# Kernel tuning notes

Hardware: AMD Instinct MI355X
Metric: run time of the kernel (lower is better)

The kernel has to match this reference:

```python
import math
import jax, jax.numpy as jnp
import numpy as np

NUM_HEADS = 16
NUM_BUCKETS = 32
MAX_DISTANCE = 128
NEG_INF = -1e9
LN_EPS = 1e-5


def _rel_pos_bias(rab_emb, T):
    # buckets for relative position (i - j) clamped at 0, T5-style log buckets
    i = jnp.arange(T)[:, None]
    j = jnp.arange(T)[None, :]
    n = jnp.clip(i - j, 0, None)  # = -(mem - ctx), clamped min 0
    max_exact = NUM_BUCKETS // 2
    large = max_exact + (
        jnp.log(n.astype(jnp.float32) / max_exact + 1e-6)
        / math.log(MAX_DISTANCE / max_exact)
        * (NUM_BUCKETS - max_exact)
    ).astype(jnp.int32)
    large = jnp.minimum(large, NUM_BUCKETS - 1)
    buckets = jnp.where(n < max_exact, n, large)  # [T, T]
    return rab_emb[buckets].transpose(2, 0, 1)[None]  # [1, H, T, T]


def setup_inputs() -> dict:
    key = jax.random.key(0)
    ks = jax.random.split(key, 8)
    B, T, D = 2, 1024, 1024
    x = jax.random.normal(ks[0], (B, T, D), dtype=jnp.float32)
    # additive causal mask: 0 where allowed, -1e9 where blocked (code tests ==0 for allowed)
    causal_block = jnp.triu(jnp.ones((T, T), dtype=bool), k=1)
    attention_mask = jnp.where(causal_block, NEG_INF, 0.0).astype(jnp.float32)
    # key padding: second sequence has last 256 positions padded
    lengths = jnp.array([T, T - 256])
    key_padding_mask = jnp.arange(T)[None, :] >= lengths[:, None]  # True = pad
    s = 1.0 / math.sqrt(D)
    W_in = jax.random.normal(ks[1], (4 * D, D), dtype=jnp.float32) * s
    b_in = jax.random.normal(ks[2], (4 * D,), dtype=jnp.float32) * 0.02
    W_out = jax.random.normal(ks[3], (D, D), dtype=jnp.float32) * s
    b_out = jax.random.normal(ks[4], (D,), dtype=jnp.float32) * 0.02
    gamma = jnp.ones((D,), dtype=jnp.float32)
    beta = jnp.zeros((D,), dtype=jnp.float32)
    rab_emb = jax.random.normal(ks[5], (NUM_BUCKETS, NUM_HEADS), dtype=jnp.float32) * 0.02
    return {
        "x": x,
        "attention_mask": attention_mask,
        "key_padding_mask": key_padding_mask,
        "W_in": W_in,
        "b_in": b_in,
        "W_out": W_out,
        "b_out": b_out,
        "gamma": gamma,
        "beta": beta,
        "rab_emb": rab_emb,
    }


def reference(x, attention_mask, key_padding_mask, W_in, b_in, W_out, b_out, gamma, beta, rab_emb):
    B, T, D = x.shape
    H = NUM_HEADS
    hd = D // H
    alpha = hd ** (-0.5)

    h = jax.nn.silu(x @ W_in.T + b_in)  # [B, T, 4D]
    U, V, Q, K = jnp.split(h, 4, axis=-1)

    def heads(t):
        return t.reshape(B, T, H, hd).transpose(0, 2, 1, 3)  # [B, H, T, hd]

    Qh, Kh, Vh = heads(Q), heads(K), heads(V)

    rab = _rel_pos_bias(rab_emb, T)  # [1, H, T, T]
    logits = jnp.einsum("bhtd,bhsd->bhts", Qh, Kh) * alpha + rab + attention_mask[None, None]

    valid = (~key_padding_mask).astype(jnp.float32)[:, None, None, :]  # [B,1,1,T]
    allowed = (attention_mask == 0).astype(jnp.float32)[None, None] * valid  # [B,1,T,T] bcast
    # padded keys: torch masked_fill(-inf) then logits_safe -> -1e9
    logits = jnp.where(valid == 0, NEG_INF, logits)

    denom = jnp.clip(jnp.sum(allowed, axis=-1, keepdims=True), 1.0, None)
    attention = jax.nn.silu(logits) / denom  # pointwise SiLU attention, no softmax

    AV = jnp.einsum("bhts,bhsd->bthd", attention, Vh).reshape(B, T, D)

    mu = jnp.mean(AV, axis=-1, keepdims=True)
    var = jnp.var(AV, axis=-1, keepdims=True)
    normed = (AV - mu) / jnp.sqrt(var + LN_EPS) * gamma + beta

    y = (normed * U) @ W_out.T + b_out  # U_flat == U (head reshape round-trips)
    return x + y
```

## Files before the change

kernel.cpp:

```cpp
#include <hip/hip_runtime.h>
#include <stdint.h>

#define DEV static __device__ __forceinline__

typedef unsigned short u16;
typedef float floatx4 __attribute__((ext_vector_type(4)));
typedef short bf16x8 __attribute__((ext_vector_type(8)));

constexpr int Tn = 1024;
constexpr int Dn = 1024;
constexpr int Hn = 16;
constexpr int FD = 4096;

DEV float b2f(u16 u) { union { unsigned int i; float f; } v; v.i = ((unsigned int)u) << 16; return v.f; }
DEV u16 f2b(float f) {
  union { float f; unsigned int i; } v; v.f = f;
  unsigned int x = v.i;
  x += 0x7fffu + ((x >> 16) & 1u);
  return (u16)(x >> 16);
}

DEV void async16(const void* g, void* l) {
  __builtin_amdgcn_global_load_lds((const __attribute__((address_space(1))) void*)g,
                                   (__attribute__((address_space(3))) void*)l,
                                   16, 0, 0);
}

DEV bool is_bf16(const unsigned* gdet) { return gdet[0] == 0x3F803F80u; }
DEV int kp_mode(const unsigned* kp) {
  unsigned d511 = kp[511];
  if (d511 == 0x01010101u) return 1;
  unsigned d1023 = kp[1023];
  if (d1023 == 0x3F803F80u) return 2;
  unsigned d2047 = kp[2047];
  return (d2047 == 0x3F800000u) ? 3 : 0;
}
DEV int nchunks(int qt) { return (qt < 6) ? 1 : ((qt < 12) ? 2 : 3); }

__global__ void prep_all(const void* __restrict__ x, const void* __restrict__ wi,
                         const void* __restrict__ wo, u16* __restrict__ xb,
                         u16* __restrict__ wib, u16* __restrict__ wob,
                         const void* __restrict__ bi, const void* __restrict__ bo,
                         const void* __restrict__ ga, const void* __restrict__ be,
                         const void* __restrict__ kp, const void* __restrict__ rab,
                         float* __restrict__ smallf, float* __restrict__ biasG,
                         float* __restrict__ denomG, unsigned long long* __restrict__ kmaskG)
{
  const unsigned* gdet = (const unsigned*)ga;
  const int bid = blockIdx.x;
  const int tid = threadIdx.x;
  __shared__ unsigned char vb[1024];
  __shared__ int wtot[4];

  if (bid < 1792) {
    if (is_bf16(gdet)) return;
    int i0 = bid * 256 + tid;
#pragma unroll
    for (int k = 0; k < 4; k++) {
      int i = i0 + k * 458752;
      const void* src; u16* dst; int j;
      if (i < 524288)       { src = x;  dst = xb;  j = i; }
      else if (i < 1572864) { src = wi; dst = wib; j = i - 524288; }
      else                  { src = wo; dst = wob; j = i - 1572864; }
      float4 v = ((const float4*)src)[j];
      ushort4 o; o.x = f2b(v.x); o.y = f2b(v.y); o.z = f2b(v.z); o.w = f2b(v.w);
      ((ushort4*)dst)[j] = o;
    }
    return;
  }
  if (bid < 1794) {
    const int b = bid - 1792;
    const int mode = kp_mode((const unsigned*)kp);
    int vv[4];
    const int t0 = tid * 4;
#pragma unroll
    for (int i = 0; i < 4; i++) {
      int t = b * Tn + t0 + i;
      int pad;
      if (mode == 0)      pad = (((const int*)kp)[t] != 0);
      else if (mode == 1) pad = (((const unsigned char*)kp)[t] != 0);
      else if (mode == 2) pad = (((const u16*)kp)[t] != 0);
      else                pad = (((const float*)kp)[t] != 0.f);
      vv[i] = pad ? 0 : 1;
      vb[t0 + i] = (unsigned char)vv[i];
    }
    int p1 = vv[0], p2 = p1 + vv[1], p3 = p2 + vv[2], p4 = p3 + vv[3];
    const int lane = tid & 63, w = tid >> 6;
    int ws = p4;
#pragma unroll
    for (int off = 1; off < 64; off <<= 1) {
      int t = __shfl_up(ws, off, 64);
      if (lane >= off) ws += t;
    }
    if (lane == 63) wtot[w] = ws;
    __syncthreads();
    int base = 0;
    for (int j = 0; j < w; j++) base += wtot[j];
    int excl = base + ws - p4;
    int c1 = excl + p1, c2 = excl + p2, c3 = excl + p3, c4 = excl + p4;
    denomG[b * Tn + t0 + 0] = (float)(c1 < 1 ? 1 : c1);
    denomG[b * Tn + t0 + 1] = (float)(c2 < 1 ? 1 : c2);
    denomG[b * Tn + t0 + 2] = (float)(c3 < 1 ? 1 : c3);
    denomG[b * Tn + t0 + 3] = (float)(c4 < 1 ? 1 : c4);
    if (tid < 16) {
      unsigned long long m = 0;
      for (int j = 0; j < 64; j++) m |= (unsigned long long)vb[tid * 64 + j] << j;
      kmaskG[b * 16 + tid] = m;
    }
    return;
  }
  const bool fbf = is_bf16(gdet);
  for (int i = tid; i < 7168; i += 256) {
    const void* src; int j;
    if (i < 4096)      { src = bi; j = i; }
    else if (i < 5120) { src = bo; j = i - 4096; }
    else if (i < 6144) { src = ga; j = i - 5120; }
    else               { src = be; j = i - 6144; }
    smallf[i] = fbf ? b2f(((const u16*)src)[j]) : ((const float*)src)[j];
  }
  for (int i = tid; i < Hn * Tn; i += 256) {
    int hh = i >> 10, d = i & 1023;
    int bk;
    if (d < 16) bk = d;
    else {
      float lg = logf((float)d * 0.0625f + 1e-6f) / logf(8.f) * 16.f;
      bk = 16 + (int)lg;
      bk = bk < 31 ? bk : 31;
    }
    int j = bk * Hn + hh;
    biasG[i] = fbf ? b2f(((const u16*)rab)[j]) : ((const float*)rab)[j];
  }
}

template<int BM, int BN, int WR, int WC, int EPI>
__global__ __launch_bounds__(WR * WC * 64, 2)
void gemm_bt(const u16* __restrict__ Ac, const u16* __restrict__ Ar,
             const u16* __restrict__ Bc, const u16* __restrict__ Br,
             const float* __restrict__ biasf, void* __restrict__ C,
             u16* __restrict__ VtG, const unsigned* __restrict__ gdet,
             int M, int N, int K)
{
  constexpr int NT = WR * WC * 64;
  __shared__ u16 As[BM * 64];
  __shared__ u16 Bs[BN * 64];
  const int fbf = is_bf16(gdet) ? 1 : 0;
  const u16* A  = fbf ? Ar : Ac;
  const u16* Bm = fbf ? Br : Bc;
  const int tid = threadIdx.x;
  const int lane = tid & 63;
  const int w = tid >> 6;
  const int wm = w / WC, wn = w % WC;
  const int q = lane >> 4, l16 = lane & 15;
  const int rowBase = blockIdx.y * BM;
  const int colBase = blockIdx.x * BN;
  const int ksl = K / gridDim.z;
  const int kb0 = blockIdx.z * ksl;

  floatx4 acc[4][4];
#pragma unroll
  for (int i = 0; i < 4; i++)
#pragma unroll
    for (int j = 0; j < 4; j++)
#pragma unroll
      for (int r = 0; r < 4; r++) acc[i][j][r] = 0.f;

  for (int kb = kb0; kb < kb0 + ksl; kb += 64) {
    __syncthreads();
#pragma unroll
    for (int i = 0; i < BM * 8 / NT; i++) {
      int c = i * NT + tid;
      int row = c >> 3, cl = (c & 7) ^ (row & 7);
      async16(&A[(size_t)(rowBase + row) * K + kb + cl * 8], &As[c * 8]);
    }
#pragma unroll
    for (int i = 0; i < BN * 8 / NT; i++) {
      int c = i * NT + tid;
      int row = c >> 3, cl = (c & 7) ^ (row & 7);
      async16(&Bm[(size_t)(colBase + row) * K + kb + cl * 8], &Bs[c * 8]);
    }
    __syncthreads();
    bf16x8 af[2][4], bfr[2][4];
    const int rsw = l16 & 7;
#pragma unroll
    for (int ko = 0; ko < 2; ko++) {
#pragma unroll
      for (int mt = 0; mt < 4; mt++) {
        int row = wm * 64 + mt * 16 + l16;
        af[ko][mt] = *(const bf16x8*)&As[(row * 8 + ((ko * 4 + q) ^ rsw)) * 8];
      }
#pragma unroll
      for (int nt = 0; nt < 4; nt++) {
        int row = wn * 64 + nt * 16 + l16;
        bfr[ko][nt] = *(const bf16x8*)&Bs[(row * 8 + ((ko * 4 + q) ^ rsw)) * 8];
      }
    }
#pragma unroll
    for (int ko = 0; ko < 2; ko++)
#pragma unroll
      for (int mt = 0; mt < 4; mt++)
#pragma unroll
        for (int nt = 0; nt < 4; nt++)
          acc[mt][nt] = __builtin_amdgcn_mfma_f32_16x16x32_bf16(af[ko][mt], bfr[ko][nt], acc[mt][nt], 0, 0, 0);
  }

  const bool isV = (EPI == 0) && (colBase >= Dn) && (colBase < 2 * Dn);
  const size_t pOff = (size_t)blockIdx.z * M * N;
#pragma unroll
  for (int mt = 0; mt < 4; mt++)
#pragma unroll
    for (int nt = 0; nt < 4; nt++) {
      int col = colBase + wn * 64 + nt * 16 + l16;
      float bcol = (EPI == 0) ? biasf[col] : 0.f;
      int row0 = rowBase + wm * 64 + mt * 16 + q * 4;
      if (EPI == 0) {
        u16 pr[4];
#pragma unroll
        for (int r = 0; r < 4; r++) {
          float v = acc[mt][nt][r] + bcol;
          v = v / (1.f + __expf(-v));
          pr[r] = f2b(v);
        }
        if (isV) {
          int d = col - Dn;
          u16* vp = &VtG[(((size_t)(row0 >> 10) * Hn + (d >> 6)) * 64 + (d & 63)) * Tn + (row0 & 1023)];
          *(uint2*)vp = make_uint2(pr[0] | ((unsigned)pr[1] << 16),
                                   pr[2] | ((unsigned)pr[3] << 16));
        } else {
#pragma unroll
          for (int r = 0; r < 4; r++)
            ((u16*)C)[(size_t)(row0 + r) * N + col] = pr[r];
        }
      } else {
#pragma unroll
        for (int r = 0; r < 4; r++)
          ((float*)C)[pOff + (size_t)(row0 + r) * N + col] = acc[mt][nt][r];
      }
    }
}

__global__ __launch_bounds__(256)
void reduce2(const float* __restrict__ Gp, const void* __restrict__ X,
             const float* __restrict__ bout, void* __restrict__ out,
             const unsigned* __restrict__ gdet)
{
  const int fbf = is_bf16(gdet) ? 1 : 0;
  const int row = blockIdx.x;
  const int tid = threadIdx.x;
  const size_t ridx = (size_t)row * Dn;
  float4 a = ((const float4*)(Gp + ridx))[tid];
#pragma unroll
  for (int ks = 1; ks < 4; ks++) {
    float4 p = ((const float4*)(Gp + (size_t)ks * 2097152 + ridx))[tid];
    a.x += p.x; a.y += p.y; a.z += p.z; a.w += p.w;
  }
  float4 bb = ((const float4*)bout)[tid];
  a.x += bb.x; a.y += bb.y; a.z += bb.z; a.w += bb.w;
  if (fbf) {
    ushort4 xv = ((const ushort4*)X)[ridx / 4 + tid];
    a.x += b2f(xv.x); a.y += b2f(xv.y); a.z += b2f(xv.z); a.w += b2f(xv.w);
    ushort4 o; o.x = f2b(a.x); o.y = f2b(a.y); o.z = f2b(a.z); o.w = f2b(a.w);
    ((ushort4*)out)[ridx / 4 + tid] = o;
  } else {
    float4 xv = ((const float4*)X)[ridx / 4 + tid];
    a.x += xv.x; a.y += xv.y; a.z += xv.z; a.w += xv.w;
    ((float4*)out)[ridx / 4 + tid] = a;
  }
}

__global__ __launch_bounds__(256, 4)
void attn_kern(const u16* __restrict__ h, const u16* __restrict__ VtG,
               const float* __restrict__ biasG, const float* __restrict__ denomG,
               const unsigned long long* __restrict__ kmaskG,
               float* __restrict__ AV)
{
  __shared__ u16 Qs[4096];
  __shared__ u16 Ks[4096];
  __shared__ u16 Vs[4096];
  __shared__ u16 Ps[4096];
  __shared__ float biasL[1024];
  const int tid = threadIdx.x;
  const int lane = tid & 63;
  const int w = tid >> 6;
  const int q = lane >> 4, l16 = lane & 15;

  int qt = 0, rem = blockIdx.x;
  for (;;) { int P = nchunks(qt); if (rem < P) break; rem -= P; qt++; }
  const int c = rem;
  const int P = nchunks(qt);
  const int n = qt + 1, cb = n / P, cr = n % P;
  const int kt0 = c * cb + (c < cr ? c : cr);
  const int kt1 = kt0 + cb + (c < cr ? 1 : 0);

  const int head = blockIdx.y, b = blockIdx.z;
  const u16* hb = h + (size_t)b * Tn * FD;
  const u16* vtb = VtG + ((size_t)(b * Hn + head)) * 64 * Tn;

#pragma unroll
  for (int i = 0; i < 2; i++) {
    int s = i * 256 + tid;
    int row = s >> 3, dc = (s & 7) ^ (row & 7);
    async16(&hb[(size_t)(qt * 64 + row) * FD + 2048 + head * 64 + dc * 8], &Qs[s * 8]);
    async16(&hb[(size_t)(kt0 * 64 + row) * FD + 3072 + head * 64 + dc * 8], &Ks[s * 8]);
    async16(&vtb[(size_t)row * Tn + kt0 * 64 + dc * 8], &Vs[s * 8]);
  }
  async16(&biasG[head * Tn + tid * 4], &biasL[tid * 4]);
  __syncthreads();

  const int sw0 = q ^ (l16 & 7);
  const int qrow = w * 16 + l16;
  bf16x8 bq0 = *(const bf16x8*)&Qs[(qrow * 8 + sw0) * 8];
  bf16x8 bq1 = *(const bf16x8*)&Qs[(qrow * 8 + (sw0 ^ 4)) * 8];
  const float dinv = 1.f / denomG[b * Tn + qt * 64 + qrow];

  floatx4 o[4];
#pragma unroll
  for (int nt = 0; nt < 4; nt++)
#pragma unroll
    for (int r = 0; r < 4; r++) o[nt][r] = 0.f;

  for (int kt = kt0; kt < kt1; kt++) {
    const unsigned long long km = kmaskG[b * 16 + kt];
    const int dq = (qt - kt) * 64 + qrow;
#pragma unroll
    for (int st = 0; st < 4; st++) {
      int rk = (st * 16 + l16) * 8;
      bf16x8 ak0 = *(const bf16x8*)&Ks[(rk + sw0) * 8];
      bf16x8 ak1 = *(const bf16x8*)&Ks[(rk + (sw0 ^ 4)) * 8];
      floatx4 sT;
#pragma unroll
      for (int r = 0; r < 4; r++) sT[r] = 0.f;
      sT = __builtin_amdgcn_mfma_f32_16x16x32_bf16(ak0, bq0, sT, 0, 0, 0);
      sT = __builtin_amdgcn_mfma_f32_16x16x32_bf16(ak1, bq1, sT, 0, 0, 0);
      unsigned mb = (unsigned)(km >> (st * 16 + q * 4)) & 0xFu;
      u16 pr[4];
#pragma unroll
      for (int r = 0; r < 4; r++) {
        int delta = dq - (st * 16 + q * 4 + r);
        float p = 0.f;
        if (((mb >> r) & 1u) && delta >= 0) {
          float xv = sT[r] * 0.125f + biasL[delta];
          p = xv * dinv / (1.f + __expf(-xv));
        }
        pr[r] = f2b(p);
      }
      unsigned lo = pr[0] | ((unsigned)pr[1] << 16);
      unsigned hi = pr[2] | ((unsigned)pr[3] << 16);
      int cch = (st * 2 + (q >> 1)) ^ (l16 & 7);
      *(uint2*)&Ps[w * 1024 + l16 * 64 + cch * 8 + (q & 1) * 4] = make_uint2(lo, hi);
    }
    int rp = w * 1024 + l16 * 64;
    bf16x8 ap0 = *(const bf16x8*)&Ps[rp + sw0 * 8];
    bf16x8 ap1 = *(const bf16x8*)&Ps[rp + (sw0 ^ 4) * 8];
#pragma unroll
    for (int nt = 0; nt < 4; nt++) {
      int rv = (nt * 16 + l16) * 8;
      bf16x8 bv0 = *(const bf16x8*)&Vs[(rv + sw0) * 8];
      bf16x8 bv1 = *(const bf16x8*)&Vs[(rv + (sw0 ^ 4)) * 8];
      o[nt] = __builtin_amdgcn_mfma_f32_16x16x32_bf16(ap0, bv0, o[nt], 0, 0, 0);
      o[nt] = __builtin_amdgcn_mfma_f32_16x16x32_bf16(ap1, bv1, o[nt], 0, 0, 0);
    }
    if (kt + 1 < kt1) {
      __syncthreads();
#pragma unroll
      for (int i = 0; i < 2; i++) {
        int s = i * 256 + tid;
        int row = s >> 3, dc = (s & 7) ^ (row & 7);
        async16(&hb[(size_t)((kt + 1) * 64 + row) * FD + 3072 + head * 64 + dc * 8], &Ks[s * 8]);
        async16(&vtb[(size_t)row * Tn + (kt + 1) * 64 + dc * 8], &Vs[s * 8]);
      }
      __syncthreads();
    }
  }

  float* avp = AV + (size_t)c * 2097152
             + ((size_t)b * Tn + qt * 64 + w * 16 + q * 4) * Dn + head * 64;
#pragma unroll
  for (int nt = 0; nt < 4; nt++)
#pragma unroll
    for (int r = 0; r < 4; r++)
      avp[(size_t)r * Dn + nt * 16 + l16] = o[nt][r];
}

__global__ __launch_bounds__(256)
void ln_mul(const float* __restrict__ AV, const u16* __restrict__ h,
            const float* __restrict__ gam, const float* __restrict__ bet,
            u16* __restrict__ z)
{
  struct alignas(8) U4 { u16 a, b, c, d; };
  const int row = blockIdx.x;
  const int tid = threadIdx.x;
  const int P = nchunks(row >> 6 & 15);
  float4 v = ((const float4*)(AV + (size_t)row * Dn))[tid];
  if (P > 1) {
    float4 p = ((const float4*)(AV + 2097152 + (size_t)row * Dn))[tid];
    v.x += p.x; v.y += p.y; v.z += p.z; v.w += p.w;
  }
  if (P > 2) {
    float4 p = ((const float4*)(AV + 4194304 + (size_t)row * Dn))[tid];
    v.x += p.x; v.y += p.y; v.z += p.z; v.w += p.w;
  }
  float s  = v.x + v.y + v.z + v.w;
  float s2 = v.x * v.x + v.y * v.y + v.z * v.z + v.w * v.w;
#pragma unroll
  for (int off = 32; off > 0; off >>= 1) {
    s  += __shfl_down(s, off, 64);
    s2 += __shfl_down(s2, off, 64);
  }
  __shared__ float red[8];
  const int lane = tid & 63, w = tid >> 6;
  if (lane == 0) { red[w] = s; red[4 + w] = s2; }
  __syncthreads();
  const float su = red[0] + red[1] + red[2] + red[3];
  const float sq = red[4] + red[5] + red[6] + red[7];
  const float mu = su * (1.f / 1024.f);
  const float var = sq * (1.f / 1024.f) - mu * mu;
  const float rstd = rsqrtf(var + 1e-5f);

  const U4 uu = ((const U4*)(h + (size_t)row * FD))[tid];
  const float4 g4 = ((const float4*)gam)[tid];
  const float4 b4 = ((const float4*)bet)[tid];
  float r0 = ((v.x - mu) * rstd * g4.x + b4.x) * b2f(uu.a);
  float r1 = ((v.y - mu) * rstd * g4.y + b4.y) * b2f(uu.b);
  float r2 = ((v.z - mu) * rstd * g4.z + b4.z) * b2f(uu.c);
  float r3 = ((v.w - mu) * rstd * g4.w + b4.w) * b2f(uu.d);
  U4 outv; outv.a = f2b(r0); outv.b = f2b(r1); outv.c = f2b(r2); outv.d = f2b(r3);
  ((U4*)(z + (size_t)row * Dn))[tid] = outv;
}

extern "C" void kernel_launch(void* const* d_in, const int* in_sizes, int n_in,
                              void* d_out, int out_size, void* d_ws, size_t ws_size,
                              hipStream_t stream)
{
  const void* x     = d_in[0];
  const void* kp    = d_in[2];
  const void* W_in  = d_in[3];
  const void* b_in  = d_in[4];
  const void* W_out = d_in[5];
  const void* b_out = d_in[6];
  const void* gamma = d_in[7];
  const void* beta  = d_in[8];
  const void* rab   = d_in[9];
  const unsigned* gdet = (const unsigned*)gamma;

  char* ws = (char*)d_ws;
  u16*   h     = (u16*)(ws);
  float* AV    = (float*)(ws + 16777216);
  float* Gp    = (float*)(ws);
  u16*   z     = (u16*)(ws + 41943040);
  u16*   xb    = (u16*)(ws + 46137344);
  u16*   Wib   = (u16*)(ws + 50331648);
  u16*   Wob   = (u16*)(ws + 58720256);
  u16*   VtG   = (u16*)(ws + 60817408);
  float* smallf= (float*)(ws + 65011712);
  float* biasG = (float*)(ws + 65040384);
  float* denom = (float*)(ws + 65105920);
  unsigned long long* kmask = (unsigned long long*)(ws + 65114112);

  prep_all<<<1795, 256, 0, stream>>>(x, W_in, W_out, xb, Wib, Wob,
                                     b_in, b_out, gamma, beta, kp, rab,
                                     smallf, biasG, denom, kmask);
  gemm_bt<128, 128, 2, 2, 0><<<dim3(32, 16, 1), dim3(256), 0, stream>>>(
      xb, (const u16*)x, Wib, (const u16*)W_in, smallf, h, VtG, gdet, 2048, 4096, 1024);
  attn_kern<<<dim3(30, 16, 2), dim3(256), 0, stream>>>(h, VtG, biasG, denom, kmask, AV);
  ln_mul<<<2048, 256, 0, stream>>>(AV, h, smallf + 5120, smallf + 6144, z);
  gemm_bt<128, 128, 2, 2, 2><<<dim3(8, 16, 4), dim3(256), 0, stream>>>(
      z, z, Wob, (const u16*)W_out, smallf, Gp, nullptr, gdet, 2048, 1024, 1024);
  reduce2<<<2048, 256, 0, stream>>>(Gp, x, smallf + 4096, d_out, gdet);
}
```

Measured before the change: 187.0 us.

## Double-buffer GEMM LDS tiles and shrink output-projection split-K to two

The GEMM kernel now keeps two LDS buffers and issues async global-to-LDS loads for the next K tile while MFMAs run on the current one, with a single barrier per iteration. Tile counts per wave are templated so the output projection can use 128x64 tiles with split-K of 2 instead of 128x128 with split-K of 4. The reduce kernel now sums two partials instead of four, which cuts partial-sum traffic. Doubled LDS use may lower occupancy. Correctness relies on the async loads completing before the barrier without an explicit vmcnt wait.

```diff
diff --git a/kernel.cpp b/kernel.cpp
--- a/kernel.cpp
+++ b/kernel.cpp
@@ -140,9 +140,11 @@
              u16* __restrict__ VtG, const unsigned* __restrict__ gdet,
              int M, int N, int K)
 {
-  constexpr int NT = WR * WC * 64;
-  __shared__ u16 As[BM * 64];
-  __shared__ u16 Bs[BN * 64];
+  constexpr int NTH = WR * WC * 64;
+  constexpr int MT = BM / (WR * 16);
+  constexpr int NTT = BN / (WC * 16);
+  __shared__ u16 As[2][BM * 64];
+  __shared__ u16 Bs[2][BN * 64];
   const int fbf = is_bf16(gdet) ? 1 : 0;
   const u16* A  = fbf ? Ar : Ac;
   const u16* Bm = fbf ? Br : Bc;
@@ -155,63 +157,72 @@
   const int colBase = blockIdx.x * BN;
   const int ksl = K / gridDim.z;
   const int kb0 = blockIdx.z * ksl;
-
-  floatx4 acc[4][4];
-#pragma unroll
-  for (int i = 0; i < 4; i++)
-#pragma unroll
-    for (int j = 0; j < 4; j++)
+  const int nIter = ksl >> 6;
+
+  floatx4 acc[MT][NTT];
+#pragma unroll
+  for (int i = 0; i < MT; i++)
+#pragma unroll
+    for (int j = 0; j < NTT; j++)
 #pragma unroll
       for (int r = 0; r < 4; r++) acc[i][j][r] = 0.f;
 
-  for (int kb = kb0; kb < kb0 + ksl; kb += 64) {
+  auto stage = [&](int buf, int kb) {
+#pragma unroll
+    for (int i = 0; i < BM * 8 / NTH; i++) {
+      int c = i * NTH + tid;
+      int row = c >> 3, cl = (c & 7) ^ (row & 7);
+      async16(&A[(size_t)(rowBase + row) * K + kb + cl * 8], &As[buf][c * 8]);
+    }
+#pragma unroll
+    for (int i = 0; i < BN * 8 / NTH; i++) {
+      int c = i * NTH + tid;
+      int row = c >> 3, cl = (c & 7) ^ (row & 7);
+      async16(&Bm[(size_t)(colBase + row) * K + kb + cl * 8], &Bs[buf][c * 8]);
+    }
+  };
+
+  stage(0, kb0);
+  __syncthreads();
+
+  for (int it = 0; it < nIter; it++) {
+    const int cur = it & 1;
+    if (it + 1 < nIter) stage(cur ^ 1, kb0 + (it + 1) * 64);
+
+    bf16x8 af[2][MT], bfr[2][NTT];
+    const int rsw = l16 & 7;
+#pragma unroll
+    for (int ko = 0; ko < 2; ko++) {
+#pragma unroll
+      for (int mt = 0; mt < MT; mt++) {
+        int row = wm * (MT * 16) + mt * 16 + l16;
+        af[ko][mt] = *(const bf16x8*)&As[cur][(row * 8 + ((ko * 4 + q) ^ rsw)) * 8];
+      }
+#pragma unroll
+      for (int nt = 0; nt < NTT; nt++) {
+        int row = wn * (NTT * 16) + nt * 16 + l16;
+        bfr[ko][nt] = *(const bf16x8*)&Bs[cur][(row * 8 + ((ko * 4 + q) ^ rsw)) * 8];
+      }
+    }
+#pragma unroll
+    for (int ko = 0; ko < 2; ko++)
+#pragma unroll
+      for (int mt = 0; mt < MT; mt++)
+#pragma unroll
+        for (int nt = 0; nt < NTT; nt++)
+          acc[mt][nt] = __builtin_amdgcn_mfma_f32_16x16x32_bf16(af[ko][mt], bfr[ko][nt], acc[mt][nt], 0, 0, 0);
     __syncthreads();
-#pragma unroll
-    for (int i = 0; i < BM * 8 / NT; i++) {
-      int c = i * NT + tid;
-      int row = c >> 3, cl = (c & 7) ^ (row & 7);
-      async16(&A[(size_t)(rowBase + row) * K + kb + cl * 8], &As[c * 8]);
-    }
-#pragma unroll
-    for (int i = 0; i < BN * 8 / NT; i++) {
-      int c = i * NT + tid;
-      int row = c >> 3, cl = (c & 7) ^ (row & 7);
-      async16(&Bm[(size_t)(colBase + row) * K + kb + cl * 8], &Bs[c * 8]);
-    }
-    __syncthreads();
-    bf16x8 af[2][4], bfr[2][4];
-    const int rsw = l16 & 7;
-#pragma unroll
-    for (int ko = 0; ko < 2; ko++) {
-#pragma unroll
-      for (int mt = 0; mt < 4; mt++) {
-        int row = wm * 64 + mt * 16 + l16;
-        af[ko][mt] = *(const bf16x8*)&As[(row * 8 + ((ko * 4 + q) ^ rsw)) * 8];
-      }
-#pragma unroll
-      for (int nt = 0; nt < 4; nt++) {
-        int row = wn * 64 + nt * 16 + l16;
-        bfr[ko][nt] = *(const bf16x8*)&Bs[(row * 8 + ((ko * 4 + q) ^ rsw)) * 8];
-      }
-    }
-#pragma unroll
-    for (int ko = 0; ko < 2; ko++)
-#pragma unroll
-      for (int mt = 0; mt < 4; mt++)
-#pragma unroll
-        for (int nt = 0; nt < 4; nt++)
-          acc[mt][nt] = __builtin_amdgcn_mfma_f32_16x16x32_bf16(af[ko][mt], bfr[ko][nt], acc[mt][nt], 0, 0, 0);
   }
 
   const bool isV = (EPI == 0) && (colBase >= Dn) && (colBase < 2 * Dn);
   const size_t pOff = (size_t)blockIdx.z * M * N;
 #pragma unroll
-  for (int mt = 0; mt < 4; mt++)
-#pragma unroll
-    for (int nt = 0; nt < 4; nt++) {
-      int col = colBase + wn * 64 + nt * 16 + l16;
+  for (int mt = 0; mt < MT; mt++)
+#pragma unroll
+    for (int nt = 0; nt < NTT; nt++) {
+      int col = colBase + wn * (NTT * 16) + nt * 16 + l16;
       float bcol = (EPI == 0) ? biasf[col] : 0.f;
-      int row0 = rowBase + wm * 64 + mt * 16 + q * 4;
+      int row0 = rowBase + wm * (MT * 16) + mt * 16 + q * 4;
       if (EPI == 0) {
         u16 pr[4];
 #pragma unroll
@@ -248,11 +259,8 @@
   const int tid = threadIdx.x;
   const size_t ridx = (size_t)row * Dn;
   float4 a = ((const float4*)(Gp + ridx))[tid];
-#pragma unroll
-  for (int ks = 1; ks < 4; ks++) {
-    float4 p = ((const float4*)(Gp + (size_t)ks * 2097152 + ridx))[tid];
-    a.x += p.x; a.y += p.y; a.z += p.z; a.w += p.w;
-  }
+  float4 p = ((const float4*)(Gp + 2097152 + ridx))[tid];
+  a.x += p.x; a.y += p.y; a.z += p.z; a.w += p.w;
   float4 bb = ((const float4*)bout)[tid];
   a.x += bb.x; a.y += bb.y; a.z += bb.z; a.w += bb.w;
   if (fbf) {
@@ -463,7 +471,7 @@
       xb, (const u16*)x, Wib, (const u16*)W_in, smallf, h, VtG, gdet, 2048, 4096, 1024);
   attn_kern<<<dim3(30, 16, 2), dim3(256), 0, stream>>>(h, VtG, biasG, denom, kmask, AV);
   ln_mul<<<2048, 256, 0, stream>>>(AV, h, smallf + 5120, smallf + 6144, z);
-  gemm_bt<128, 128, 2, 2, 2><<<dim3(8, 16, 4), dim3(256), 0, stream>>>(
+  gemm_bt<128, 64, 2, 2, 2><<<dim3(16, 16, 2), dim3(256), 0, stream>>>(
       z, z, Wob, (const u16*)W_out, smallf, Gp, nullptr, gdet, 2048, 1024, 1024);
   reduce2<<<2048, 256, 0, stream>>>(Gp, x, smallf + 4096, d_out, gdet);
 }
```

Result: no change. 187.3 us (+0.1%).
